# Performance work log

Measured on AMD Instinct MI355X. Metric: run time of the kernel, lower is better.

The kernel has to match this reference:

```python
import jax, jax.numpy as jnp
import numpy as np

N = 50000   # num_nodes
E = 250000  # edges per view
D = 128     # in_dim = h_dim = out_dim
B = 4       # num_bases
RELS = (8, 12, 6)


def setup_inputs() -> dict:
    key = jax.random.key(0)
    ks = iter(jax.random.split(key, 64))
    s = 1.0 / np.sqrt(D)
    inp = {"node_features": jax.random.normal(next(ks), (N, D), jnp.float32) * 0.1}
    for v, R in enumerate(RELS, start=1):
        inp[f"src{v}"] = jax.random.randint(next(ks), (E,), 0, N)
        inp[f"dst{v}"] = jax.random.randint(next(ks), (E,), 0, N)
        inp[f"rel{v}"] = jax.random.randint(next(ks), (E,), 0, R)
        for l in (1, 2):
            inp[f"v{v}_bases{l}"] = jax.random.normal(next(ks), (B, D, D), jnp.float32) * s
            inp[f"v{v}_coef{l}"] = jax.random.normal(next(ks), (R, B), jnp.float32) * 0.5
            inp[f"v{v}_loopw{l}"] = jax.random.normal(next(ks), (D, D), jnp.float32) * s
            inp[f"v{v}_bias{l}"] = jnp.zeros((D,), jnp.float32)
    inp["fusion_w"] = jax.random.normal(next(ks), (3 * D, D), jnp.float32) * (1.0 / np.sqrt(3 * D))
    inp["fusion_b"] = jnp.zeros((D,), jnp.float32)
    return inp


def rgcn_layer(h, src, dst, rel, bases, coef, loop_w, bias, act):
    # basis trick: project nodes through all bases once, then combine per edge
    node_proj = jnp.einsum('ni,bio->nbo', h, bases)          # [N,B,out]
    msg = jnp.einsum('eb,ebo->eo', coef[rel], node_proj[src])  # [E,out]
    agg = jax.ops.segment_sum(msg, dst, num_segments=h.shape[0])
    out = agg + h @ loop_w + bias                             # self-loop + bias (DGL defaults)
    return jax.nn.relu(out) if act else out


def single_view(feats, src, dst, rel, bases1, coef1, loopw1, bias1,
                bases2, coef2, loopw2, bias2):
    h = rgcn_layer(feats, src, dst, rel, bases1, coef1, loopw1, bias1, act=True)
    return rgcn_layer(h, src, dst, rel, bases2, coef2, loopw2, bias2, act=False)


def reference(node_features,
              src1, dst1, rel1, src2, dst2, rel2, src3, dst3, rel3,
              v1_bases1, v1_coef1, v1_loopw1, v1_bias1,
              v1_bases2, v1_coef2, v1_loopw2, v1_bias2,
              v2_bases1, v2_coef1, v2_loopw1, v2_bias1,
              v2_bases2, v2_coef2, v2_loopw2, v2_bias2,
              v3_bases1, v3_coef1, v3_loopw1, v3_bias1,
              v3_bases2, v3_coef2, v3_loopw2, v3_bias2,
              fusion_w, fusion_b):
    h1 = single_view(node_features, src1, dst1, rel1,
                     v1_bases1, v1_coef1, v1_loopw1, v1_bias1,
                     v1_bases2, v1_coef2, v1_loopw2, v1_bias2)
    h2 = single_view(node_features, src2, dst2, rel2,
                     v2_bases1, v2_coef1, v2_loopw1, v2_bias1,
                     v2_bases2, v2_coef2, v2_loopw2, v2_bias2)
    h3 = single_view(node_features, src3, dst3, rel3,
                     v3_bases1, v3_coef1, v3_loopw1, v3_bias1,
                     v3_bases2, v3_coef2, v3_loopw2, v3_bias2)
    h_cat = jnp.concatenate([h1, h2, h3], axis=-1)  # [N, 3*D]
    return h_cat @ fusion_w + fusion_b
```

## Files before the change

kernel.cpp:

```cpp
#include <hip/hip_runtime.h>
#include <hip/hip_bf16.h>
#include <stdint.h>

typedef _Float16 f16x8 __attribute__((ext_vector_type(8)));
typedef _Float16 f16x2 __attribute__((ext_vector_type(2)));
typedef float f32x4 __attribute__((ext_vector_type(4)));


__device__ __forceinline__ void gll16(const _Float16* g, _Float16* l) {
    __builtin_amdgcn_global_load_lds(
        (const __attribute__((address_space(1))) void*)g,
        (__attribute__((address_space(3))) void*)l, 16, 0, 0);
}

struct PrepDesc { const float* src; _Float16* dst; int dstride; };
struct PrepArgs { PrepDesc d[33]; };

__global__ __launch_bounds__(256) void prep_weights(PrepArgs args) {
    __shared__ _Float16 lds[128 * 129];
    const PrepDesc de = args.d[blockIdx.x];
    int t = threadIdx.x;
    for (int q = 0; q < 64; ++q) {
        int li = t + q * 256;
        int i = li >> 7, o = li & 127;
        lds[o * 129 + i] = (_Float16)de.src[li];
    }
    __syncthreads();
    for (int q = 0; q < 64; ++q) {
        int lo = t + q * 256;
        int o = lo >> 7, i = lo & 127;
        de.dst[(size_t)o * de.dstride + (i ^ ((o & 7) << 3))] = lds[o * 129 + i];
    }
}

struct FoldArgs {
    const float* bases2[3];
    const float* loopw2[3];
    const float* fw;
    const float* b2[3];
    const float* fb;
    _Float16* W2F[3];
    float* bias_out;
};

__global__ __launch_bounds__(256) void fold_w2f(FoldArgs fa) {
    int c = blockIdx.x, v = blockIdx.y, t = threadIdx.x;
    if (c == 5) {
        if (v != 0) return;
        __shared__ float s[256];
        int of = t & 127, half = t >> 7;
        float acc = 0.f;
        for (int j = half * 192; j < (half + 1) * 192; ++j)
            acc += fa.b2[j >> 7][j & 127] * fa.fw[(size_t)j * 128 + of];
        s[t] = acc;
        __syncthreads();
        if (half == 0) fa.bias_out[of] = fa.fb[of] + s[of] + s[of + 128];
        return;
    }
    __shared__ _Float16 As[128 * 136];
    __shared__ _Float16 Bs[128 * 136];
    const float* A = (c < 4) ? fa.bases2[v] + (size_t)c * 16384 : fa.loopw2[v];
    for (int q = 0; q < 64; ++q) {
        int li = t + q * 256;
        int i = li >> 7, o2 = li & 127;
        As[i * 136 + o2] = (_Float16)A[li];
    }
    for (int q = 0; q < 64; ++q) {
        int li = t + q * 256;
        int o2 = li >> 7, of = li & 127;
        Bs[of * 136 + o2] = (_Float16)fa.fw[(size_t)(v * 128 + o2) * 128 + of];
    }
    __syncthreads();

    int wid = t >> 6, lane = t & 63;
    int wr = (wid >> 1) * 64;
    int wc = (wid & 1) * 64;
    int lm = lane & 15;
    int lk = (lane >> 4) * 8;

    f32x4 acc[4][4] = {};
    for (int ks = 0; ks < 4; ++ks) {
        f16x8 a[4], b[4];
        for (int mi = 0; mi < 4; ++mi)
            a[mi] = *(const f16x8*)(As + (wr + mi * 16 + lm) * 136 + ks * 32 + lk);
        for (int ni = 0; ni < 4; ++ni)
            b[ni] = *(const f16x8*)(Bs + (wc + ni * 16 + lm) * 136 + ks * 32 + lk);
        for (int mi = 0; mi < 4; ++mi)
            for (int ni = 0; ni < 4; ++ni)
                acc[mi][ni] = __builtin_amdgcn_mfma_f32_16x16x32_f16(a[mi], b[ni], acc[mi][ni], 0, 0, 0);
    }

    int rbase = (lane >> 4) * 4;
    _Float16* dst = fa.W2F[v];
    for (int mi = 0; mi < 4; ++mi) {
        for (int j = 0; j < 4; ++j) {
            int i = wr + mi * 16 + rbase + j;
            for (int ni = 0; ni < 4; ++ni) {
                int of = wc + ni * 16 + lm;
                dst[(size_t)of * 640 + c * 128 + (i ^ ((of & 7) << 3))] = (_Float16)acc[mi][ni][j];
            }
        }
    }
}

__global__ __launch_bounds__(256) void f32_to_f16(const float* __restrict__ in,
                                                  _Float16* __restrict__ out, int n4) {
    int i = blockIdx.x * 256 + threadIdx.x;
    if (i >= n4) return;
    float4 v = *((const float4*)in + i);
    int n = i >> 5;
    int c = (i & 31) * 4;
    int cs = c ^ ((n & 7) << 3);
    f16x2 a, b;
    a[0] = (_Float16)v.x; a[1] = (_Float16)v.y;
    b[0] = (_Float16)v.z; b[1] = (_Float16)v.w;
    _Float16* o = out + (size_t)n * 128 + cs;
    *(f16x2*)o = a;
    *(f16x2*)(o + 2) = b;
}

struct EdgeArgs {
    const int* src[3]; const int* dst[3]; const int* rel[3];
    int E[3]; int N;
};

__global__ __launch_bounds__(256) void bhist(EdgeArgs ea, int* __restrict__ hmat, int nbk) {
    __shared__ int cnt[256];
    int v = blockIdx.y, blk = blockIdx.x, t = threadIdx.x;
    cnt[t] = 0;
    __syncthreads();
    int E = ea.E[v];
    const int* dst = ea.dst[v];
    int chunk = (E + 63) >> 6;
    int e0 = blk * chunk;
    int e1 = min(e0 + chunk, E);
    for (int e = e0 + t; e < e1; e += 256)
        atomicAdd(&cnt[dst[e] >> 8], 1);
    __syncthreads();
    if (t < nbk)
        hmat[((size_t)v * nbk + t) * 64 + blk] = cnt[t];
}

__global__ __launch_bounds__(256) void scan1_kernel(const int* __restrict__ deg,
                                                    int* __restrict__ off,
                                                    int* __restrict__ bsum, int n) {
    __shared__ int s[256];
    int b = blockIdx.x, t = threadIdx.x;
    int base = b * 2048 + t * 8;
    int v[8]; int sum = 0;
    for (int j = 0; j < 8; ++j) {
        int x = (base + j < n) ? deg[base + j] : 0;
        v[j] = sum;
        sum += x;
    }
    s[t] = sum;
    __syncthreads();
    for (int st = 1; st < 256; st <<= 1) {
        int y = (t >= st) ? s[t - st] : 0;
        __syncthreads();
        s[t] += y;
        __syncthreads();
    }
    int texcl = t ? s[t - 1] : 0;
    if (t == 255) bsum[b] = s[255];
    for (int j = 0; j < 8; ++j)
        if (base + j < n) off[base + j] = texcl + v[j];
}

__device__ __forceinline__ int chunk_pref(const int* bsum, int flat) {
    int ck = flat >> 11;
    int p = 0;
    for (int j = 0; j < ck; ++j) p += bsum[j];
    return p;
}

__global__ __launch_bounds__(256) void bscat(EdgeArgs ea, const int* __restrict__ smat,
                                             const int* __restrict__ bsum,
                                             int* __restrict__ mid, int nbk) {
    __shared__ int cur[256];
    int v = blockIdx.y, blk = blockIdx.x, t = threadIdx.x;
    if (t < nbk) {
        int flat = ((size_t)v * nbk + t) * 64 + blk;
        cur[t] = smat[flat] + chunk_pref(bsum, flat);
    }
    __syncthreads();
    int E = ea.E[v];
    const int* src = ea.src[v];
    const int* dst = ea.dst[v];
    const int* rel = ea.rel[v];
    int chunk = (E + 63) >> 6;
    int e0 = blk * chunk;
    int e1 = min(e0 + chunk, E);
    for (int e = e0 + t; e < e1; e += 256) {
        int d = dst[e];
        int pos = atomicAdd(&cur[d >> 8], 1);
        mid[pos] = src[e] | (rel[e] << 16) | ((d & 255) << 20);
    }
}

__global__ __launch_bounds__(256) void bfinal(const int* __restrict__ smat,
                                              const int* __restrict__ bsum,
                                              const int* __restrict__ mid,
                                              int* __restrict__ off3,
                                              int* __restrict__ packed3,
                                              int M, int nbk, int Etot) {
    __shared__ int cnt[256];
    __shared__ int s[256];
    __shared__ int cur[256];
    int bk = blockIdx.x, v = blockIdx.y, t = threadIdx.x;
    int flat0 = (v * nbk + bk) * 64;
    int flat1 = flat0 + 64;
    int nflat = 3 * nbk * 64;
    int start = smat[flat0] + chunk_pref(bsum, flat0);
    int end   = (flat1 < nflat) ? smat[flat1] + chunk_pref(bsum, flat1) : Etot;
    cnt[t] = 0;
    __syncthreads();
    for (int i = start + t; i < end; i += 256)
        atomicAdd(&cnt[(mid[i] >> 20) & 255], 1);
    __syncthreads();
    s[t] = cnt[t];
    __syncthreads();
    for (int st = 1; st < 256; st <<= 1) {
        int y = (t >= st) ? s[t - st] : 0;
        __syncthreads();
        s[t] += y;
        __syncthreads();
    }
    int excl = t ? s[t - 1] : 0;
    int node = (bk << 8) + t;
    if (node < M) off3[(size_t)v * M + node] = start + excl;
    cur[t] = start + excl;
    __syncthreads();
    for (int i = start + t; i < end; i += 256) {
        int m = mid[i];
        int pos = atomicAdd(&cur[(m >> 20) & 255], 1);
        packed3[pos] = (m & 0xFFFF) | (((m >> 16) & 15) << 20);
    }
    if (v == 2 && bk == nbk - 1 && t == 0) off3[(size_t)3 * M] = Etot;
}

struct GatherArgs {
    const int* off3;
    const int* packed3;
    const float* coef[3];
    const _Float16* h[3];
    _Float16* T;
    int N; size_t Tvs;
};

__global__ __launch_bounds__(256) void gather3(GatherArgs g) {
    int v = blockIdx.y;
    int wid = threadIdx.x >> 6;
    int lane = threadIdx.x & 63;
    int nodeA = blockIdx.x * 8 + wid * 2;
    if (nodeA >= g.N) return;
    int nodeB = nodeA + 1;
    bool hasB = nodeB < g.N;

    const int* off = g.off3 + (size_t)v * g.N;
    const float* coef = g.coef[v];
    const _Float16* h = g.h[v];
    _Float16* T = g.T + (size_t)v * g.Tvs;

    int iA = __builtin_amdgcn_readfirstlane(off[nodeA]);
    int eA = __builtin_amdgcn_readfirstlane(off[nodeA + 1]);
    int iB = eA;
    int eB = hasB ? __builtin_amdgcn_readfirstlane(off[nodeB + 1]) : eA;

    float accA[8] = {}, accB[8] = {};

    auto edge1 = [&](int p, float* acc) {
        int s = p & 0xFFFFF, r = p >> 20;
        uint32_t q = ((const uint32_t*)(h + (size_t)s * 128))[lane ^ ((s & 7) << 2)];
        float4 c = *(const float4*)(coef + (size_t)r * 4);
        f16x2 u = __builtin_bit_cast(f16x2, q);
        float lo = (float)u[0], hi = (float)u[1];
        acc[0] += c.x * lo;  acc[1] += c.x * hi;
        acc[2] += c.y * lo;  acc[3] += c.y * hi;
        acc[4] += c.z * lo;  acc[5] += c.z * hi;
        acc[6] += c.w * lo;  acc[7] += c.w * hi;
    };

    for (; iA + 1 < eA && iB + 1 < eB; iA += 2, iB += 2) {
        int pA0 = __builtin_amdgcn_readfirstlane(g.packed3[iA]);
        int pA1 = __builtin_amdgcn_readfirstlane(g.packed3[iA + 1]);
        int pB0 = __builtin_amdgcn_readfirstlane(g.packed3[iB]);
        int pB1 = __builtin_amdgcn_readfirstlane(g.packed3[iB + 1]);
        int sA0 = pA0 & 0xFFFFF, sA1 = pA1 & 0xFFFFF;
        int sB0 = pB0 & 0xFFFFF, sB1 = pB1 & 0xFFFFF;
        uint32_t qA0 = ((const uint32_t*)(h + (size_t)sA0 * 128))[lane ^ ((sA0 & 7) << 2)];
        uint32_t qA1 = ((const uint32_t*)(h + (size_t)sA1 * 128))[lane ^ ((sA1 & 7) << 2)];
        uint32_t qB0 = ((const uint32_t*)(h + (size_t)sB0 * 128))[lane ^ ((sB0 & 7) << 2)];
        uint32_t qB1 = ((const uint32_t*)(h + (size_t)sB1 * 128))[lane ^ ((sB1 & 7) << 2)];
        float4 cA0 = *(const float4*)(coef + (size_t)(pA0 >> 20) * 4);
        float4 cA1 = *(const float4*)(coef + (size_t)(pA1 >> 20) * 4);
        float4 cB0 = *(const float4*)(coef + (size_t)(pB0 >> 20) * 4);
        float4 cB1 = *(const float4*)(coef + (size_t)(pB1 >> 20) * 4);
        f16x2 u;
        float lo, hi;
        u = __builtin_bit_cast(f16x2, qA0); lo = (float)u[0]; hi = (float)u[1];
        accA[0] += cA0.x * lo; accA[1] += cA0.x * hi; accA[2] += cA0.y * lo; accA[3] += cA0.y * hi;
        accA[4] += cA0.z * lo; accA[5] += cA0.z * hi; accA[6] += cA0.w * lo; accA[7] += cA0.w * hi;
        u = __builtin_bit_cast(f16x2, qA1); lo = (float)u[0]; hi = (float)u[1];
        accA[0] += cA1.x * lo; accA[1] += cA1.x * hi; accA[2] += cA1.y * lo; accA[3] += cA1.y * hi;
        accA[4] += cA1.z * lo; accA[5] += cA1.z * hi; accA[6] += cA1.w * lo; accA[7] += cA1.w * hi;
        u = __builtin_bit_cast(f16x2, qB0); lo = (float)u[0]; hi = (float)u[1];
        accB[0] += cB0.x * lo; accB[1] += cB0.x * hi; accB[2] += cB0.y * lo; accB[3] += cB0.y * hi;
        accB[4] += cB0.z * lo; accB[5] += cB0.z * hi; accB[6] += cB0.w * lo; accB[7] += cB0.w * hi;
        u = __builtin_bit_cast(f16x2, qB1); lo = (float)u[0]; hi = (float)u[1];
        accB[0] += cB1.x * lo; accB[1] += cB1.x * hi; accB[2] += cB1.y * lo; accB[3] += cB1.y * hi;
        accB[4] += cB1.z * lo; accB[5] += cB1.z * hi; accB[6] += cB1.w * lo; accB[7] += cB1.w * hi;
    }
    for (; iA + 1 < eA; iA += 2) {
        int p0 = __builtin_amdgcn_readfirstlane(g.packed3[iA]);
        int p1 = __builtin_amdgcn_readfirstlane(g.packed3[iA + 1]);
        edge1(p0, accA); edge1(p1, accA);
    }
    for (; iA < eA; ++iA)
        edge1(__builtin_amdgcn_readfirstlane(g.packed3[iA]), accA);
    for (; iB + 1 < eB; iB += 2) {
        int p0 = __builtin_amdgcn_readfirstlane(g.packed3[iB]);
        int p1 = __builtin_amdgcn_readfirstlane(g.packed3[iB + 1]);
        edge1(p0, accB); edge1(p1, accB);
    }
    for (; iB < eB; ++iB)
        edge1(__builtin_amdgcn_readfirstlane(g.packed3[iB]), accB);

    {
        int cs = (2 * lane) ^ ((nodeA & 7) << 3);
        _Float16* tb = T + (size_t)nodeA * 512 + cs;
        for (int b = 0; b < 4; ++b) {
            f16x2 o; o[0] = (_Float16)accA[2 * b]; o[1] = (_Float16)accA[2 * b + 1];
            *(f16x2*)(tb + b * 128) = o;
        }
    }
    if (hasB) {
        int cs = (2 * lane) ^ ((nodeB & 7) << 3);
        _Float16* tb = T + (size_t)nodeB * 512 + cs;
        for (int b = 0; b < 4; ++b) {
            f16x2 o; o[0] = (_Float16)accB[2 * b]; o[1] = (_Float16)accB[2 * b + 1];
            *(f16x2*)(tb + b * 128) = o;
        }
    }
}

struct GemmArgs {
    const _Float16* T;
    const _Float16* hin[3];
    const _Float16* WT[3];
    const float* bias[3];
    _Float16* hout;
    int M; int relu; size_t Tvs; size_t hovs;
};

__global__ __launch_bounds__(512) void gemm_layer(GemmArgs ga) {
    __shared__ _Float16 As[64 * 128];
    __shared__ _Float16 Bs[128 * 128];
    int v = blockIdx.y;
    const _Float16* Tb  = ga.T + (size_t)v * ga.Tvs;
    const _Float16* hin = ga.hin[v];
    const _Float16* BT  = ga.WT[v];
    const float* bias   = ga.bias[v];
    _Float16* out       = ga.hout + (size_t)v * ga.hovs;
    int M = ga.M;

    int tid = threadIdx.x;
    int m0 = blockIdx.x * 64;
    int wid = tid >> 6, lane = tid & 63;
    int wr = (wid >> 2) * 32;
    int wc = (wid & 3) * 32;
    int lm = lane & 15;
    int lk = (lane >> 4) * 8;
    int xm = (lm & 7) << 3;

    f32x4 acc[2][2] = {};

    for (int kb = 0; kb < 5; ++kb) {
        const _Float16* Asrc; size_t astride;
        if (kb < 4) { Asrc = Tb + (size_t)kb * 128; astride = 512; }
        else        { Asrc = hin;                   astride = 128; }
        for (int q = 0; q < 2; ++q) {
            int li = tid + q * 512;
            int r = li >> 4;
            int c = (li & 15) << 3;
            int gr = m0 + r; if (gr >= M) gr = M - 1;
            gll16(Asrc + (size_t)gr * astride + c, As + (size_t)li * 8);
        }
        for (int q = 0; q < 4; ++q) {
            int li = tid + q * 512;
            gll16(BT + (size_t)(li >> 4) * 640 + kb * 128 + ((li & 15) << 3),
                  Bs + (size_t)li * 8);
        }
        __syncthreads();

        for (int ks = 0; ks < 4; ++ks) {
            int ac = (ks * 32 + lk) ^ xm;
            f16x8 a[2], b[2];
            for (int mi = 0; mi < 2; ++mi)
                a[mi] = *(const f16x8*)(As + (wr + mi * 16 + lm) * 128 + ac);
            for (int ni = 0; ni < 2; ++ni)
                b[ni] = *(const f16x8*)(Bs + (wc + ni * 16 + lm) * 128 + ac);
            for (int mi = 0; mi < 2; ++mi)
                for (int ni = 0; ni < 2; ++ni)
                    acc[mi][ni] = __builtin_amdgcn_mfma_f32_16x16x32_f16(a[mi], b[ni], acc[mi][ni], 0, 0, 0);
        }
        __syncthreads();
    }

    int rbase = (lane >> 4) * 4;
    for (int mi = 0; mi < 2; ++mi) {
        for (int j = 0; j < 4; ++j) {
            int gr = m0 + wr + mi * 16 + rbase + j;
            if (gr >= M) continue;
            int rs = (gr & 7) << 3;
            for (int ni = 0; ni < 2; ++ni) {
                int col = wc + ni * 16 + lm;
                float val = acc[mi][ni][j] + bias[col];
                if (ga.relu) val = fmaxf(val, 0.f);
                out[(size_t)gr * 128 + (col ^ rs)] = (_Float16)val;
            }
        }
    }
}

struct L2FArgs {
    const _Float16* T;
    const _Float16* h1;
    const _Float16* W2F[3];
    const float* bias;
    float* out; int M; size_t Tvs; size_t hvs;
};

__global__ __launch_bounds__(512) void gemm_l2f(L2FArgs ga) {
    __shared__ _Float16 As[64 * 128];
    __shared__ _Float16 Bs[128 * 128];
    int M = ga.M;
    int tid = threadIdx.x;
    int m0 = blockIdx.x * 64;
    int wid = tid >> 6, lane = tid & 63;
    int wr = (wid >> 2) * 32;
    int wc = (wid & 3) * 32;
    int lm = lane & 15;
    int lk = (lane >> 4) * 8;
    int xm = (lm & 7) << 3;

    f32x4 acc[2][2] = {};

    for (int v = 0; v < 3; ++v) {
        const _Float16* Tb = ga.T + (size_t)v * ga.Tvs;
        const _Float16* hb = ga.h1 + (size_t)v * ga.hvs;
        const _Float16* BT = ga.W2F[v];
        for (int kb = 0; kb < 5; ++kb) {
            const _Float16* Asrc; size_t astride;
            if (kb < 4) { Asrc = Tb + (size_t)kb * 128; astride = 512; }
            else        { Asrc = hb;                    astride = 128; }
            for (int q = 0; q < 2; ++q) {
                int li = tid + q * 512;
                int r = li >> 4;
                int c = (li & 15) << 3;
                int gr = m0 + r; if (gr >= M) gr = M - 1;
                gll16(Asrc + (size_t)gr * astride + c, As + (size_t)li * 8);
            }
            for (int q = 0; q < 4; ++q) {
                int li = tid + q * 512;
                gll16(BT + (size_t)(li >> 4) * 640 + kb * 128 + ((li & 15) << 3),
                      Bs + (size_t)li * 8);
            }
            __syncthreads();

            for (int ks = 0; ks < 4; ++ks) {
                int ac = (ks * 32 + lk) ^ xm;
                f16x8 a[2], b[2];
                for (int mi = 0; mi < 2; ++mi)
                    a[mi] = *(const f16x8*)(As + (wr + mi * 16 + lm) * 128 + ac);
                for (int ni = 0; ni < 2; ++ni)
                    b[ni] = *(const f16x8*)(Bs + (wc + ni * 16 + lm) * 128 + ac);
                for (int mi = 0; mi < 2; ++mi)
                    for (int ni = 0; ni < 2; ++ni)
                        acc[mi][ni] = __builtin_amdgcn_mfma_f32_16x16x32_f16(a[mi], b[ni], acc[mi][ni], 0, 0, 0);
            }
            __syncthreads();
        }
    }

    int rbase = (lane >> 4) * 4;
    for (int mi = 0; mi < 2; ++mi) {
        for (int j = 0; j < 4; ++j) {
            int gr = m0 + wr + mi * 16 + rbase + j;
            if (gr >= M) continue;
            for (int ni = 0; ni < 2; ++ni) {
                int col = wc + ni * 16 + lm;
                ga.out[(size_t)gr * 128 + col] = acc[mi][ni][j] + ga.bias[col];
            }
        }
    }
}

extern "C" void kernel_launch(void* const* d_in, const int* in_sizes, int n_in,
                              void* d_out, int out_size, void* d_ws, size_t ws_size,
                              hipStream_t stream) {
    const int D = 128;
    const int M = in_sizes[0] / D;

    struct ViewIn {
        const int *src, *dst, *rel;
        const float *bases1, *coef1, *loopw1, *bias1;
        const float *bases2, *coef2, *loopw2, *bias2;
        int E;
    } V[3];
    int idx = 1;
    for (int v = 0; v < 3; ++v) {
        V[v].src    = (const int*)d_in[idx + 0];
        V[v].dst    = (const int*)d_in[idx + 1];
        V[v].rel    = (const int*)d_in[idx + 2];
        V[v].bases1 = (const float*)d_in[idx + 3];
        V[v].coef1  = (const float*)d_in[idx + 4];
        V[v].loopw1 = (const float*)d_in[idx + 5];
        V[v].bias1  = (const float*)d_in[idx + 6];
        V[v].bases2 = (const float*)d_in[idx + 7];
        V[v].coef2  = (const float*)d_in[idx + 8];
        V[v].loopw2 = (const float*)d_in[idx + 9];
        V[v].bias2  = (const float*)d_in[idx + 10];
        V[v].E      = in_sizes[idx + 0];
        idx += 11;
    }
    const float* fusion_w = (const float*)d_in[idx];
    const float* fusion_b = (const float*)d_in[idx + 1];
    int Etot = V[0].E + V[1].E + V[2].E;

    int nbk = (M + 255) >> 8;
    int nsc = 3 * nbk * 64;

    char* w = (char*)d_ws;
    auto alloc = [&](size_t bytes) -> char* {
        char* p = w; w += (bytes + 255) & ~(size_t)255; return p;
    };
    _Float16* nf16 = (_Float16*)alloc((size_t)M * 128 * 2);
    _Float16* wts  = (_Float16*)alloc((size_t)(3 * 81920) * 2);
    _Float16* w2f  = (_Float16*)alloc((size_t)(3 * 81920) * 2);
    float* bias_o  = (float*)alloc(128 * 4);
    int* hmat      = (int*)alloc((size_t)nsc * 4);
    int* smat      = (int*)alloc(((size_t)nsc + 1) * 4);
    int* bsum      = (int*)alloc(512);
    int* off3      = (int*)alloc(((size_t)3 * M + 1) * 4);
    int* mid       = (int*)alloc((size_t)Etot * 4);
    int* packed3   = (int*)alloc((size_t)Etot * 4);
    _Float16* T3   = (_Float16*)alloc((size_t)3 * M * 512 * 2);
    _Float16* h1b  = (_Float16*)alloc((size_t)3 * M * 128 * 2);

    _Float16 *WT1[3], *W2F[3];
    for (int v = 0; v < 3; ++v) {
        WT1[v] = wts + (size_t)v * 81920;
        W2F[v] = w2f + (size_t)v * 81920;
    }

    PrepArgs pa;
    int t = 0;
    for (int v = 0; v < 3; ++v) {
        for (int b = 0; b < 4; ++b) {
            pa.d[t].src = V[v].bases1 + (size_t)b * 16384;
            pa.d[t].dst = WT1[v] + (size_t)b * 128;
            pa.d[t].dstride = 640; ++t;
        }
        pa.d[t].src = V[v].loopw1;
        pa.d[t].dst = WT1[v] + 512;
        pa.d[t].dstride = 640; ++t;
    }
    prep_weights<<<t, 256, 0, stream>>>(pa);

    FoldArgs fo;
    for (int v = 0; v < 3; ++v) {
        fo.bases2[v] = V[v].bases2;
        fo.loopw2[v] = V[v].loopw2;
        fo.W2F[v] = W2F[v];
        fo.b2[v] = V[v].bias2;
    }
    fo.fw = fusion_w;
    fo.fb = fusion_b;
    fo.bias_out = bias_o;
    fold_w2f<<<dim3(6, 3), 256, 0, stream>>>(fo);

    int n4 = M * D / 4;
    f32_to_f16<<<(n4 + 255) / 256, 256, 0, stream>>>((const float*)d_in[0], nf16, n4);

    EdgeArgs ea;
    for (int v = 0; v < 3; ++v) {
        ea.src[v] = V[v].src; ea.dst[v] = V[v].dst; ea.rel[v] = V[v].rel; ea.E[v] = V[v].E;
    }
    ea.N = M;
    int nsb = (nsc + 2047) / 2048;
    bhist<<<dim3(64, 3), 256, 0, stream>>>(ea, hmat, nbk);
    scan1_kernel<<<nsb, 256, 0, stream>>>(hmat, smat, bsum, nsc);
    bscat<<<dim3(64, 3), 256, 0, stream>>>(ea, smat, bsum, mid, nbk);
    bfinal<<<dim3(nbk, 3), 256, 0, stream>>>(smat, bsum, mid, off3, packed3, M, nbk, Etot);

    int ng  = (M + 7) / 8;
    int gxL = (M + 63) / 64;
    size_t Tvs = (size_t)M * 512;
    size_t hvs = (size_t)M * 128;
    float* outF = (float*)d_out;

    GatherArgs g1;
    g1.off3 = off3; g1.packed3 = packed3; g1.T = T3; g1.N = M; g1.Tvs = Tvs;
    for (int v = 0; v < 3; ++v) { g1.coef[v] = V[v].coef1; g1.h[v] = nf16; }
    gather3<<<dim3(ng, 3), 256, 0, stream>>>(g1);

    GemmArgs m1;
    m1.T = T3; m1.hout = h1b; m1.M = M; m1.relu = 1; m1.Tvs = Tvs; m1.hovs = hvs;
    for (int v = 0; v < 3; ++v) { m1.hin[v] = nf16; m1.WT[v] = WT1[v]; m1.bias[v] = V[v].bias1; }
    gemm_layer<<<dim3(gxL, 3), 512, 0, stream>>>(m1);

    GatherArgs g2 = g1;
    for (int v = 0; v < 3; ++v) { g2.coef[v] = V[v].coef2; g2.h[v] = h1b + (size_t)v * hvs; }
    gather3<<<dim3(ng, 3), 256, 0, stream>>>(g2);

    L2FArgs l2;
    l2.T = T3; l2.h1 = h1b; l2.bias = bias_o; l2.out = outF;
    l2.M = M; l2.Tvs = Tvs; l2.hvs = hvs;
    for (int v = 0; v < 3; ++v) l2.W2F[v] = W2F[v];
    gemm_l2f<<<gxL, 512, 0, stream>>>(l2);
}
```

Baseline: 285.3 us.

## Double-buffer LDS tiles with async prefetch in the layer and fusion GEMMs

Both MFMA GEMM kernels now use two LDS buffers holding 64-wide K slices instead of one 128-wide slice. The loads for step kb+2 are issued right after step kb's compute, and explicit vmcnt waits plus raw s_barrier replace the previous load, sync, compute, sync loop. This is meant to hide global-to-LDS latency behind the MFMA work. The cost is twice as many loop iterations and hand-written waitcnt logic that relies on exactly three loads being issued per stage.

Measured after the change: 286.9 us. Within noise of the previous version (+0.6%).

```diff
diff --git a/kernel.cpp b/kernel.cpp
--- a/kernel.cpp
+++ b/kernel.cpp
@@ -354,8 +354,8 @@
 };
 
 __global__ __launch_bounds__(512) void gemm_layer(GemmArgs ga) {
-    __shared__ _Float16 As[64 * 128];
-    __shared__ _Float16 Bs[128 * 128];
+    __shared__ _Float16 As[2][64 * 64];
+    __shared__ _Float16 Bs[2][128 * 64];
     int v = blockIdx.y;
     const _Float16* Tb  = ga.T + (size_t)v * ga.Tvs;
     const _Float16* hin = ga.hin[v];
@@ -373,38 +373,45 @@
     int lk = (lane >> 4) * 8;
     int xm = (lm & 7) << 3;
 
-    f32x4 acc[2][2] = {};
-
-    for (int kb = 0; kb < 5; ++kb) {
-        const _Float16* Asrc; size_t astride;
-        if (kb < 4) { Asrc = Tb + (size_t)kb * 128; astride = 512; }
-        else        { Asrc = hin;                   astride = 128; }
+    int ar = tid >> 3, acs = (tid & 7) << 3;
+    int agr = m0 + ar; if (agr >= M) agr = M - 1;
+
+    auto stage = [&](int kb, int pb) {
+        const _Float16* Asrc; size_t astride; int acb;
+        if (kb < 8) { Asrc = Tb;  astride = 512; acb = kb * 64; }
+        else        { Asrc = hin; astride = 128; acb = (kb - 8) * 64; }
+        gll16(Asrc + (size_t)agr * astride + acb + acs, &As[pb][tid * 8]);
+        int gcb = kb * 64;
         for (int q = 0; q < 2; ++q) {
             int li = tid + q * 512;
-            int r = li >> 4;
-            int c = (li & 15) << 3;
-            int gr = m0 + r; if (gr >= M) gr = M - 1;
-            gll16(Asrc + (size_t)gr * astride + c, As + (size_t)li * 8);
-        }
-        for (int q = 0; q < 4; ++q) {
-            int li = tid + q * 512;
-            gll16(BT + (size_t)(li >> 4) * 640 + kb * 128 + ((li & 15) << 3),
-                  Bs + (size_t)li * 8);
-        }
-        __syncthreads();
-
-        for (int ks = 0; ks < 4; ++ks) {
+            int r = li >> 3, c = (li & 7) << 3;
+            gll16(BT + (size_t)r * 640 + gcb + c, &Bs[pb][(size_t)li * 8]);
+        }
+    };
+
+    f32x4 acc[2][2] = {};
+    stage(0, 0);
+    stage(1, 1);
+
+    for (int kb = 0; kb < 10; ++kb) {
+        if (kb >= 8) { asm volatile("s_waitcnt vmcnt(0)" ::: "memory"); }
+        else         { asm volatile("s_waitcnt vmcnt(3)" ::: "memory"); }
+        __builtin_amdgcn_sched_barrier(0);
+        __builtin_amdgcn_s_barrier();
+        int pb = kb & 1;
+        for (int ks = 0; ks < 2; ++ks) {
             int ac = (ks * 32 + lk) ^ xm;
             f16x8 a[2], b[2];
             for (int mi = 0; mi < 2; ++mi)
-                a[mi] = *(const f16x8*)(As + (wr + mi * 16 + lm) * 128 + ac);
+                a[mi] = *(const f16x8*)(&As[pb][(wr + mi * 16 + lm) * 64 + ac]);
             for (int ni = 0; ni < 2; ++ni)
-                b[ni] = *(const f16x8*)(Bs + (wc + ni * 16 + lm) * 128 + ac);
+                b[ni] = *(const f16x8*)(&Bs[pb][(wc + ni * 16 + lm) * 64 + ac]);
             for (int mi = 0; mi < 2; ++mi)
                 for (int ni = 0; ni < 2; ++ni)
                     acc[mi][ni] = __builtin_amdgcn_mfma_f32_16x16x32_f16(a[mi], b[ni], acc[mi][ni], 0, 0, 0);
         }
-        __syncthreads();
+        __builtin_amdgcn_s_barrier();
+        if (kb + 2 < 10) stage(kb + 2, pb);
     }
 
     int rbase = (lane >> 4) * 4;
@@ -432,8 +439,8 @@
 };
 
 __global__ __launch_bounds__(512) void gemm_l2f(L2FArgs ga) {
-    __shared__ _Float16 As[64 * 128];
-    __shared__ _Float16 Bs[128 * 128];
+    __shared__ _Float16 As[2][64 * 64];
+    __shared__ _Float16 Bs[2][128 * 64];
     int M = ga.M;
     int tid = threadIdx.x;
     int m0 = blockIdx.x * 64;
@@ -444,43 +451,48 @@
     int lk = (lane >> 4) * 8;
     int xm = (lm & 7) << 3;
 
+    int ar = tid >> 3, acs = (tid & 7) << 3;
+    int agr = m0 + ar; if (agr >= M) agr = M - 1;
+
+    auto stage = [&](int kb, int pb) {
+        int v = kb / 10;
+        int lkb = kb - v * 10;
+        const _Float16* Asrc; size_t astride; int acb;
+        if (lkb < 8) { Asrc = ga.T + (size_t)v * ga.Tvs;  astride = 512; acb = lkb * 64; }
+        else         { Asrc = ga.h1 + (size_t)v * ga.hvs; astride = 128; acb = (lkb - 8) * 64; }
+        gll16(Asrc + (size_t)agr * astride + acb + acs, &As[pb][tid * 8]);
+        const _Float16* BT = ga.W2F[v];
+        int gcb = lkb * 64;
+        for (int q = 0; q < 2; ++q) {
+            int li = tid + q * 512;
+            int r = li >> 3, c = (li & 7) << 3;
+            gll16(BT + (size_t)r * 640 + gcb + c, &Bs[pb][(size_t)li * 8]);
+        }
+    };
+
     f32x4 acc[2][2] = {};
-
-    for (int v = 0; v < 3; ++v) {
-        const _Float16* Tb = ga.T + (size_t)v * ga.Tvs;
-        const _Float16* hb = ga.h1 + (size_t)v * ga.hvs;
-        const _Float16* BT = ga.W2F[v];
-        for (int kb = 0; kb < 5; ++kb) {
-            const _Float16* Asrc; size_t astride;
-            if (kb < 4) { Asrc = Tb + (size_t)kb * 128; astride = 512; }
-            else        { Asrc = hb;                    astride = 128; }
-            for (int q = 0; q < 2; ++q) {
-                int li = tid + q * 512;
-                int r = li >> 4;
-                int c = (li & 15) << 3;
-                int gr = m0 + r; if (gr >= M) gr = M - 1;
-                gll16(Asrc + (size_t)gr * astride + c, As + (size_t)li * 8);
-            }
-            for (int q = 0; q < 4; ++q) {
-                int li = tid + q * 512;
-                gll16(BT + (size_t)(li >> 4) * 640 + kb * 128 + ((li & 15) << 3),
-                      Bs + (size_t)li * 8);
-            }
-            __syncthreads();
-
-            for (int ks = 0; ks < 4; ++ks) {
-                int ac = (ks * 32 + lk) ^ xm;
-                f16x8 a[2], b[2];
-                for (int mi = 0; mi < 2; ++mi)
-                    a[mi] = *(const f16x8*)(As + (wr + mi * 16 + lm) * 128 + ac);
+    stage(0, 0);
+    stage(1, 1);
+
+    for (int kb = 0; kb < 30; ++kb) {
+        if (kb >= 28) { asm volatile("s_waitcnt vmcnt(0)" ::: "memory"); }
+        else          { asm volatile("s_waitcnt vmcnt(3)" ::: "memory"); }
+        __builtin_amdgcn_sched_barrier(0);
+        __builtin_amdgcn_s_barrier();
+        int pb = kb & 1;
+        for (int ks = 0; ks < 2; ++ks) {
+            int ac = (ks * 32 + lk) ^ xm;
+            f16x8 a[2], b[2];
+            for (int mi = 0; mi < 2; ++mi)
+                a[mi] = *(const f16x8*)(&As[pb][(wr + mi * 16 + lm) * 64 + ac]);
+            for (int ni = 0; ni < 2; ++ni)
+                b[ni] = *(const f16x8*)(&Bs[pb][(wc + ni * 16 + lm) * 64 + ac]);
+            for (int mi = 0; mi < 2; ++mi)
                 for (int ni = 0; ni < 2; ++ni)
-                    b[ni] = *(const f16x8*)(Bs + (wc + ni * 16 + lm) * 128 + ac);
-                for (int mi = 0; mi < 2; ++mi)
-                    for (int ni = 0; ni < 2; ++ni)
-                        acc[mi][ni] = __builtin_amdgcn_mfma_f32_16x16x32_f16(a[mi], b[ni], acc[mi][ni], 0, 0, 0);
-            }
-            __syncthreads();
-        }
+                    acc[mi][ni] = __builtin_amdgcn_mfma_f32_16x16x32_f16(a[mi], b[ni], acc[mi][ni], 0, 0, 0);
+        }
+        __builtin_amdgcn_s_barrier();
+        if (kb + 2 < 30) stage(kb + 2, pb);
     }
 
     int rbase = (lane >> 4) * 4;
```
